# Kernel optimization log

Measured on AMD Instinct MI355X. Metric: run time of the kernel, lower is better.

The kernel has to match this reference:

```python
import jax, jax.numpy as jnp
import numpy as np
from jax import lax

BN_EPS = 1e-5


def _conv_bn_relu(x, W, b, gamma, beta):
    # x: [B, Cin, N]; W: [Cout, Cin]; 1x1 conv == channel GEMM
    y = jnp.einsum('oc,bcn->bon', W, x) + b[None, :, None]
    mean = jnp.mean(y, axis=(0, 2), keepdims=True)
    var = jnp.mean((y - mean) ** 2, axis=(0, 2), keepdims=True)  # biased, torch BN train mode
    y = gamma[None, :, None] * (y - mean) / jnp.sqrt(var + BN_EPS) + beta[None, :, None]
    return jax.nn.relu(y)


def setup_inputs() -> dict:
    key = jax.random.key(0)
    ks = jax.random.split(key, 8)
    B, N1, N2, C1, C2 = 16, 4096, 1024, 128, 256
    Cin, H = C1 + C2, 256  # MLP dims [384, 256, 256]
    inp = {
        'centroids1': jax.random.normal(ks[0], (B, 3, N1), jnp.float32),
        'centroids2': jax.random.normal(ks[1], (B, 3, N2), jnp.float32),
        'features1': jax.random.normal(ks[2], (B, C1, N1), jnp.float32),
        'features2': jax.random.normal(ks[3], (B, C2, N2), jnp.float32),
        'W1': jax.random.normal(ks[4], (H, Cin), jnp.float32) / np.sqrt(Cin),
        'b1': jnp.zeros((H,), jnp.float32),
        'g1': jnp.ones((H,), jnp.float32),
        'be1': jnp.zeros((H,), jnp.float32),
        'W2': jax.random.normal(ks[5], (H, H), jnp.float32) / np.sqrt(H),
        'b2': jnp.zeros((H,), jnp.float32),
        'g2': jnp.ones((H,), jnp.float32),
        'be2': jnp.zeros((H,), jnp.float32),
    }
    return inp


def reference(centroids1, centroids2, features1, features2,
              W1, b1, g1, be1, W2, b2, g2, be2):
    c1 = centroids1.transpose(0, 2, 1)  # [B, N1, 3]
    c2 = centroids2.transpose(0, 2, 1)  # [B, N2, 3]
    f2 = features2.transpose(0, 2, 1)   # [B, N2, C2]

    # pairwise squared distances [B, N1, N2]
    d = (jnp.sum(c1 ** 2, -1)[:, :, None] + jnp.sum(c2 ** 2, -1)[:, None, :]
         - 2.0 * jnp.einsum('bnd,bmd->bnm', c1, c2))

    # 3 nearest neighbors (smallest distances)
    neg_top, idx = lax.top_k(-d, 3)            # idx: [B, N1, 3]
    dist3 = -neg_top
    recip = 1.0 / (dist3 + 1e-8)
    weight = recip / jnp.sum(recip, axis=2, keepdims=True)  # [B, N1, 3]

    gathered = jax.vmap(lambda f, i: f[i])(f2, idx)         # [B, N1, 3, C2]
    interp = jnp.sum(gathered * weight[..., None], axis=2)  # [B, N1, C2]

    feats = jnp.concatenate((features1.transpose(0, 2, 1), interp), axis=-1)  # [B, N1, C1+C2]
    x = feats.transpose(0, 2, 1)  # [B, C1+C2, N1]
    x = _conv_bn_relu(x, W1, b1, g1, be1)
    x = _conv_bn_relu(x, W2, b2, g2, be2)
    return x  # [B, 256, N1]
```

## Files before the change

kernel.cpp:

```cpp
#include <hip/hip_runtime.h>
#include <math.h>

#define N1 4096
#define N2 1024
#define C1 128
#define C2 256
#define CIN 384
#define H 256
#define BATCH 16
#define BN_EPS 1e-5f

typedef __attribute__((ext_vector_type(8))) short bf16x8;
typedef __attribute__((ext_vector_type(4))) float f32x4;

__device__ inline float bf2f(short s) {
    union { unsigned u; float f; } x;
    x.u = ((unsigned)(unsigned short)s) << 16;
    return x.f;
}
__device__ inline short f2bf(float f) {
    union { float f; unsigned u; } x; x.f = f;
    unsigned r = x.u + 0x7fffu + ((x.u >> 16) & 1u);
    return (short)(r >> 16);
}

__global__ __launch_bounds__(256)
void knn_kernel(const float* __restrict__ c1, const float* __restrict__ c2,
                float4* __restrict__ pk) {
    __shared__ __align__(16) float4 sc[N2];
    __shared__ float md[64 * 13];
    __shared__ int   mi[64 * 13];
    const int b = blockIdx.y;
    const float* c2b = c2 + (size_t)b * 3 * N2;
    for (int j = threadIdx.x; j < N2; j += 256) {
        float xx = c2b[j], yy = c2b[N2 + j], zz = c2b[2 * N2 + j];
        sc[j] = make_float4(xx, yy, zz, xx * xx + yy * yy + zz * zz);
    }
    __syncthreads();

    const int t = threadIdx.x;
    const int q = t & 63;
    const int quarter = t >> 6;
    const int n = blockIdx.x * 64 + q;
    const float* c1b = c1 + (size_t)b * 3 * N1;
    const float x = c1b[n], y = c1b[N1 + n], z = c1b[2 * N1 + n];
    const float s1 = x * x + y * y + z * z;

    float d0 = 3.4e38f, d1 = 3.4e38f, d2 = 3.4e38f;
    int i0 = 0, i1 = 0, i2 = 0;
    const int j0 = quarter * 256;
    #pragma unroll 8
    for (int jj = 0; jj < 256; ++jj) {
        const int j = j0 + jj;
        float4 cc = sc[j];
        float dot = x * cc.x + y * cc.y + z * cc.z;
        float d = s1 + cc.w - 2.0f * dot;
        bool c0v = d < d0, c1v = d < d1, c2v = d < d2;
        i2 = c1v ? i1 : (c2v ? j : i2);
        i1 = c0v ? i0 : (c1v ? j : i1);
        i0 = c0v ? j  : i0;
        d2 = __builtin_amdgcn_fmed3f(d1, d2, d);
        d1 = __builtin_amdgcn_fmed3f(d0, d1, d);
        d0 = fminf(d0, d);
    }
    const int mb = q * 13 + quarter * 3;
    md[mb + 0] = d0; md[mb + 1] = d1; md[mb + 2] = d2;
    mi[mb + 0] = i0; mi[mb + 1] = i1; mi[mb + 2] = i2;
    __syncthreads();

    if (t < 64) {
        float e0 = 3.4e38f, e1 = 3.4e38f, e2 = 3.4e38f;
        int a0 = 0, a1 = 0, a2 = 0;
        #pragma unroll
        for (int r = 0; r < 12; ++r) {
            const int rr = t * 13 + (r / 3) * 3 + (r % 3);
            float d = md[rr]; int j = mi[rr];
            bool c0 = d < e0, c1v = d < e1, c2v = d < e2;
            e2 = c1v ? e1 : (c2v ? d : e2);  a2 = c1v ? a1 : (c2v ? j : a2);
            e1 = c0 ? e0 : (c1v ? d : e1);   a1 = c0 ? a0 : (c1v ? j : a1);
            e0 = c0 ? d  : e0;               a0 = c0 ? j  : a0;
        }
        float r0 = 1.0f / (e0 + 1e-8f);
        float r1 = 1.0f / (e1 + 1e-8f);
        float r2 = 1.0f / (e2 + 1e-8f);
        float rs = r0 + r1 + r2;
        unsigned pack = (unsigned)a0 | ((unsigned)a1 << 10) | ((unsigned)a2 << 20);
        pk[(size_t)b * N1 + n] = make_float4(__uint_as_float(pack), r0 / rs, r1 / rs, r2 / rs);
    }
}

__global__ __launch_bounds__(256)
void prep_w(const float* __restrict__ W, short* __restrict__ Wsw, int K) {
    const int nkb = K >> 3;
    const int id = blockIdx.x * 256 + threadIdx.x;
    if (id >= 256 * nkb) return;
    const int m = id / nkb, kb = id % nkb;
    const float* src = W + (size_t)m * K + kb * 8;
    bf16x8 v;
    #pragma unroll
    for (int j = 0; j < 8; ++j) v[j] = f2bf(src[j]);
    *(bf16x8*)(Wsw + ((size_t)kb * 256 + m) * 8) = v;
}

__global__ __launch_bounds__(256)
void transpose_f2(const float* __restrict__ f2, short* __restrict__ f2t) {
    __shared__ float st[32][33];
    const int j0 = blockIdx.x * 32, c0 = blockIdx.y * 32, b = blockIdx.z;
    const int t = threadIdx.x;
    {
        const int cc = t >> 3, jj = (t & 7) * 4;
        const float* src = f2 + ((size_t)b * C2 + c0 + cc) * N2 + j0 + jj;
        float4 v = *(const float4*)src;
        st[cc][jj + 0] = v.x; st[cc][jj + 1] = v.y;
        st[cc][jj + 2] = v.z; st[cc][jj + 3] = v.w;
    }
    __syncthreads();
    {
        const int j = t >> 3, cb = (t & 7) * 4;
        short4 v = { f2bf(st[cb + 0][j]), f2bf(st[cb + 1][j]),
                     f2bf(st[cb + 2][j]), f2bf(st[cb + 3][j]) };
        *(short4*)(f2t + ((size_t)b * N2 + j0 + j) * C2 + c0 + cb) = v;
    }
}

__global__ __launch_bounds__(256)
void prep_B1(const short* __restrict__ f2t, const float4* __restrict__ pk,
             short* __restrict__ B1) {
    const int b = blockIdx.y;
    const int n = blockIdx.x * 256 + threadIdx.x;
    float4 v = pk[(size_t)b * N1 + n];
    unsigned u = __float_as_uint(v.x);
    const short* r0 = f2t + ((size_t)b * N2 + (u & 1023u)) * C2;
    const short* r1 = f2t + ((size_t)b * N2 + ((u >> 10) & 1023u)) * C2;
    const short* r2 = f2t + ((size_t)b * N2 + ((u >> 20) & 1023u)) * C2;
    short* ob = B1 + ((size_t)b * 32 * N1 + n) * 8;
    #pragma unroll 4
    for (int kb = 0; kb < 32; ++kb) {
        bf16x8 g0 = *(const bf16x8*)(r0 + kb * 8);
        bf16x8 g1 = *(const bf16x8*)(r1 + kb * 8);
        bf16x8 g2 = *(const bf16x8*)(r2 + kb * 8);
        bf16x8 o;
        #pragma unroll
        for (int e = 0; e < 8; ++e)
            o[e] = f2bf(fmaf(v.w, bf2f(g2[e]), fmaf(v.z, bf2f(g1[e]), v.y * bf2f(g0[e]))));
        *(bf16x8*)(ob + (size_t)kb * N1 * 8) = o;
    }
}

template<int MODE>
__global__ __launch_bounds__(256, 4)
void gemm_kernel(const short* __restrict__ Wsw,
                 const float* __restrict__ f1, const short* __restrict__ Bkc,
                 const float* __restrict__ scale, const float* __restrict__ shift,
                 short* __restrict__ Ykc, float2* __restrict__ P) {
    __shared__ float sc_s[256], sh_s[256];
    __shared__ float2 pb[128][2];

    const int t = threadIdx.x;
    const int d = blockIdx.x;
    const int grp = d >> 4, rem = d & 15;
    const int mh = rem >> 3;
    const int pair = grp * 8 + (rem & 7);
    const int nt = pair & 31, b = pair >> 5;
    const int n0 = nt * 128;

    const int lane = t & 63, wv = t >> 6;
    const int wm = wv >> 1, wn = wv & 1;
    const int l16 = lane & 15, lq = lane >> 4;

    if (MODE == 1) {
        sc_s[t] = scale[t]; sh_s[t] = shift[t];
        __syncthreads();
    }

    const short* Bb = Bkc + (size_t)b * 32 * N1 * 8;
    const short* Abase = Wsw + ((size_t)lq * 256 + mh * 128 + wm * 64 + l16) * 8;
    const int nfr = n0 + wn * 64 + l16;

    f32x4 acc[4][4];
    #pragma unroll
    for (int i = 0; i < 4; ++i)
        #pragma unroll
        for (int j = 0; j < 4; ++j)
            acc[i][j] = (f32x4){0.f, 0.f, 0.f, 0.f};

    if (MODE == 0) {
        const float* f1b = f1 + (size_t)b * C1 * N1;
        #pragma unroll
        for (int s = 0; s < 4; ++s) {
            bf16x8 a[4], bv[4];
            const short* ap = Abase + (size_t)s * 4 * 256 * 8;
            #pragma unroll
            for (int f = 0; f < 4; ++f) a[f] = *(const bf16x8*)(ap + f * 16 * 8);
            const float* fp = f1b + (size_t)(s * 32 + lq * 8) * N1 + nfr;
            #pragma unroll
            for (int f = 0; f < 4; ++f) {
                #pragma unroll
                for (int e = 0; e < 8; ++e)
                    bv[f][e] = f2bf(fp[(size_t)e * N1 + f * 16]);
            }
            #pragma unroll
            for (int i = 0; i < 4; ++i)
                #pragma unroll
                for (int j = 0; j < 4; ++j)
                    acc[i][j] = __builtin_amdgcn_mfma_f32_16x16x32_bf16(a[i], bv[j], acc[i][j], 0, 0, 0);
        }
        #pragma unroll
        for (int s = 4; s < 12; ++s) {
            bf16x8 a[4], bv[4];
            const short* ap = Abase + (size_t)s * 4 * 256 * 8;
            #pragma unroll
            for (int f = 0; f < 4; ++f) a[f] = *(const bf16x8*)(ap + f * 16 * 8);
            const short* bp = Bb + ((size_t)(s * 4 + lq - 16) * N1 + nfr) * 8;
            #pragma unroll
            for (int f = 0; f < 4; ++f) bv[f] = *(const bf16x8*)(bp + f * 16 * 8);
            #pragma unroll
            for (int i = 0; i < 4; ++i)
                #pragma unroll
                for (int j = 0; j < 4; ++j)
                    acc[i][j] = __builtin_amdgcn_mfma_f32_16x16x32_bf16(a[i], bv[j], acc[i][j], 0, 0, 0);
        }
    } else {
        #pragma unroll
        for (int s = 0; s < 8; ++s) {
            bf16x8 a[4], raw[4], bv[4];
            const short* ap = Abase + (size_t)s * 4 * 256 * 8;
            #pragma unroll
            for (int f = 0; f < 4; ++f) a[f] = *(const bf16x8*)(ap + f * 16 * 8);
            const short* bp = Bb + ((size_t)(s * 4 + lq) * N1 + nfr) * 8;
            #pragma unroll
            for (int f = 0; f < 4; ++f) raw[f] = *(const bf16x8*)(bp + f * 16 * 8);
            const int k0 = s * 32 + lq * 8;
            float sck[8], shk[8];
            #pragma unroll
            for (int e = 0; e < 8; ++e) { sck[e] = sc_s[k0 + e]; shk[e] = sh_s[k0 + e]; }
            #pragma unroll
            for (int f = 0; f < 4; ++f)
                #pragma unroll
                for (int e = 0; e < 8; ++e)
                    bv[f][e] = f2bf(fmaxf(fmaf(bf2f(raw[f][e]), sck[e], shk[e]), 0.f));
            #pragma unroll
            for (int i = 0; i < 4; ++i)
                #pragma unroll
                for (int j = 0; j < 4; ++j)
                    acc[i][j] = __builtin_amdgcn_mfma_f32_16x16x32_bf16(a[i], bv[j], acc[i][j], 0, 0, 0);
        }
    }

    short* Yb = Ykc + (size_t)b * 32 * N1 * 8;
    #pragma unroll
    for (int i = 0; i < 4; ++i) {
        const int kb = mh * 16 + wm * 8 + i * 2 + (lq >> 1);
        const int kr0 = (lq & 1) * 4;
        #pragma unroll
        for (int j = 0; j < 4; ++j) {
            const int n = n0 + wn * 64 + j * 16 + l16;
            short4 v = { f2bf(acc[i][j][0]), f2bf(acc[i][j][1]),
                         f2bf(acc[i][j][2]), f2bf(acc[i][j][3]) };
            *(short4*)(Yb + ((size_t)kb * N1 + n) * 8 + kr0) = v;
        }
    }

    #pragma unroll
    for (int i = 0; i < 4; ++i) {
        #pragma unroll
        for (int r = 0; r < 4; ++r) {
            float s = 0.f, qq = 0.f;
            #pragma unroll
            for (int j = 0; j < 4; ++j) {
                float xv = acc[i][j][r];
                s += xv; qq += xv * xv;
            }
            #pragma unroll
            for (int msk = 1; msk < 16; msk <<= 1) {
                s  += __shfl_xor(s, msk);
                qq += __shfl_xor(qq, msk);
            }
            if (l16 == 0)
                pb[wm * 64 + i * 16 + lq * 4 + r][wn] = make_float2(s, qq);
        }
    }
    __syncthreads();
    if (t < 128) {
        float2 a = pb[t][0], c = pb[t][1];
        P[(size_t)(mh * 128 + t) * 512 + b * 32 + nt] = make_float2(a.x + c.x, a.y + c.y);
    }
}

__global__ __launch_bounds__(256)
void bn_reduce(const float2* __restrict__ P, const float* __restrict__ g,
               const float* __restrict__ be, float* __restrict__ scale,
               float* __restrict__ shift) {
    const int c = blockIdx.x, t = threadIdx.x;
    float2 v0 = P[(size_t)c * 512 + t];
    float2 v1 = P[(size_t)c * 512 + 256 + t];
    float s = v0.x + v1.x, q = v0.y + v1.y;
    __shared__ float ss[256], sq[256];
    ss[t] = s; sq[t] = q;
    __syncthreads();
    for (int o = 128; o > 0; o >>= 1) {
        if (t < o) { ss[t] += ss[t + o]; sq[t] += sq[t + o]; }
        __syncthreads();
    }
    if (t == 0) {
        const float inv = 1.0f / (float)(BATCH * N1);
        float mean = ss[0] * inv;
        float var  = sq[0] * inv - mean * mean;
        float sc = g[c] / sqrtf(var + BN_EPS);
        scale[c] = sc;
        shift[c] = be[c] - mean * sc;
    }
}

__global__ __launch_bounds__(256)
void final_bn_relu(const short* __restrict__ y2kc, const float* __restrict__ scale,
                   const float* __restrict__ shift, float* __restrict__ out) {
    const int t = threadIdx.x;
    const int n0 = blockIdx.x * 1024 + t * 4;
    const int kb = blockIdx.y, b = blockIdx.z;
    const short* src = y2kc + ((size_t)(b * 32 + kb) * N1 + n0) * 8;
    bf16x8 v0 = *(const bf16x8*)(src);
    bf16x8 v1 = *(const bf16x8*)(src + 8);
    bf16x8 v2 = *(const bf16x8*)(src + 16);
    bf16x8 v3 = *(const bf16x8*)(src + 24);
    #pragma unroll
    for (int e = 0; e < 8; ++e) {
        const float sc = scale[kb * 8 + e], sh = shift[kb * 8 + e];
        float4 o;
        o.x = fmaxf(fmaf(bf2f(v0[e]), sc, sh), 0.f);
        o.y = fmaxf(fmaf(bf2f(v1[e]), sc, sh), 0.f);
        o.z = fmaxf(fmaf(bf2f(v2[e]), sc, sh), 0.f);
        o.w = fmaxf(fmaf(bf2f(v3[e]), sc, sh), 0.f);
        *(float4*)(out + ((size_t)(b * 256 + kb * 8 + e) * N1) + n0) = o;
    }
}

extern "C" void kernel_launch(void* const* d_in, const int* in_sizes, int n_in,
                              void* d_out, int out_size, void* d_ws, size_t ws_size,
                              hipStream_t stream) {
    const float* c1  = (const float*)d_in[0];
    const float* c2  = (const float*)d_in[1];
    const float* f1  = (const float*)d_in[2];
    const float* f2  = (const float*)d_in[3];
    const float* W1  = (const float*)d_in[4];
    const float* g1  = (const float*)d_in[6];
    const float* be1 = (const float*)d_in[7];
    const float* W2  = (const float*)d_in[8];
    const float* g2  = (const float*)d_in[10];
    const float* be2 = (const float*)d_in[11];
    float* out = (float*)d_out;

    char* ws = (char*)d_ws;
    short*  B1   = (short*)ws;
    short*  y2kc = (short*)ws;
    short*  f2t  = (short*)(ws + (32u << 20));
    short*  y1kc = (short*)(ws + (32u << 20));
    short*  W1s  = (short*)(ws + (64u << 20));
    short*  W2s  = (short*)(ws + (64u << 20) + (256u << 10));
    float4* pk   = (float4*)(ws + (64u << 20) + (512u << 10));
    float2* P    = (float2*)(ws + (64u << 20) + (512u << 10) + (1u << 20));
    float* scale1 = (float*)(ws + (64u << 20) + (512u << 10) + (2u << 20));
    float* shift1 = scale1 + 256;
    float* scale2 = shift1 + 256;
    float* shift2 = scale2 + 256;

    prep_w<<<48, 256, 0, stream>>>(W1, W1s, CIN);
    prep_w<<<32, 256, 0, stream>>>(W2, W2s, H);
    transpose_f2<<<dim3(N2 / 32, C2 / 32, BATCH), 256, 0, stream>>>(f2, f2t);
    knn_kernel<<<dim3(N1 / 64, BATCH), 256, 0, stream>>>(c1, c2, pk);
    prep_B1<<<dim3(N1 / 256, BATCH), 256, 0, stream>>>(f2t, pk, B1);

    gemm_kernel<0><<<1024, 256, 0, stream>>>(
        W1s, f1, B1, nullptr, nullptr, y1kc, P);
    bn_reduce<<<256, 256, 0, stream>>>(P, g1, be1, scale1, shift1);

    gemm_kernel<1><<<1024, 256, 0, stream>>>(
        W2s, nullptr, y1kc, scale1, shift1, y2kc, P);
    bn_reduce<<<256, 256, 0, stream>>>(P, g2, be2, scale2, shift2);

    final_bn_relu<<<dim3(N1 / 1024, 32, BATCH), 256, 0, stream>>>(y2kc, scale2, shift2, out);
}
```

Before: 151.4 us.

## Stage GEMM operands through double-buffered LDS with async global-to-LDS loads

After: 165.6 us. +9.4%, slower.

```diff
diff --git a/kernel.cpp b/kernel.cpp
--- a/kernel.cpp
+++ b/kernel.cpp
@@ -22,6 +22,12 @@
     union { float f; unsigned u; } x; x.f = f;
     unsigned r = x.u + 0x7fffu + ((x.u >> 16) & 1u);
     return (short)(r >> 16);
+}
+
+typedef const __attribute__((address_space(1))) unsigned int guint;
+typedef __attribute__((address_space(3))) unsigned int luint;
+__device__ inline void gll16(const void* g, void* l) {
+    __builtin_amdgcn_global_load_lds((guint*)g, (luint*)l, 16, 0, 0);
 }
 
 __global__ __launch_bounds__(256)
@@ -148,12 +154,15 @@
 }
 
 template<int MODE>
-__global__ __launch_bounds__(256, 4)
+__global__ __launch_bounds__(256)
 void gemm_kernel(const short* __restrict__ Wsw,
                  const float* __restrict__ f1, const short* __restrict__ Bkc,
-                 const float* __restrict__ scale, const float* __restrict__ shift,
                  short* __restrict__ Ykc, float2* __restrict__ P) {
-    __shared__ float sc_s[256], sh_s[256];
+    constexpr int K = (MODE == 0) ? CIN : H;
+    constexpr int NT = K / 32;
+
+    __shared__ __align__(16) short A_lds[2][4][128][8];
+    __shared__ __align__(16) short B_lds[2][4][128][8];
     __shared__ float2 pb[128][2];
 
     const int t = threadIdx.x;
@@ -168,14 +177,11 @@
     const int wm = wv >> 1, wn = wv & 1;
     const int l16 = lane & 15, lq = lane >> 4;
 
-    if (MODE == 1) {
-        sc_s[t] = scale[t]; sh_s[t] = shift[t];
-        __syncthreads();
-    }
-
+    const float* f1b = (MODE == 0) ? f1 + (size_t)b * C1 * N1 : (const float*)nullptr;
     const short* Bb = Bkc + (size_t)b * 32 * N1 * 8;
-    const short* Abase = Wsw + ((size_t)lq * 256 + mh * 128 + wm * 64 + l16) * 8;
-    const int nfr = n0 + wn * 64 + l16;
+
+    const int skb = t >> 7;
+    const int sn0 = t & 127;
 
     f32x4 acc[4][4];
     #pragma unroll
@@ -184,67 +190,85 @@
         for (int j = 0; j < 4; ++j)
             acc[i][j] = (f32x4){0.f, 0.f, 0.f, 0.f};
 
+    auto stageA = [&](int step, int bufi) {
+        #pragma unroll
+        for (int i = 0; i < 2; ++i) {
+            const int u0 = i * 256 + wv * 64;
+            const int kb = u0 >> 7, m0 = u0 & 127;
+            const short* g = Wsw + (((size_t)step * 4 + kb) * 256 + mh * 128 + m0 + lane) * 8;
+            gll16(g, &A_lds[bufi][0][0][0] + (size_t)u0 * 8);
+        }
+    };
+    auto stageB_gll = [&](int kbg, int bufi) {
+        #pragma unroll
+        for (int i = 0; i < 2; ++i) {
+            const int u0 = i * 256 + wv * 64;
+            const int kb = u0 >> 7, nn = u0 & 127;
+            const short* g = Bb + (((size_t)(kbg + kb)) * N1 + n0 + nn + lane) * 8;
+            gll16(g, &B_lds[bufi][0][0][0] + (size_t)u0 * 8);
+        }
+    };
+
+    float pf[16];
+    auto loadF1 = [&](int step) {
+        #pragma unroll
+        for (int h = 0; h < 2; ++h) {
+            const int kb = skb + h * 2;
+            const float* src = f1b + (size_t)(step * 32 + kb * 8) * N1 + n0 + sn0;
+            #pragma unroll
+            for (int e = 0; e < 8; ++e) pf[h * 8 + e] = src[(size_t)e * N1];
+        }
+    };
+    auto writeF1 = [&](int bufi) {
+        #pragma unroll
+        for (int h = 0; h < 2; ++h) {
+            const int kb = skb + h * 2;
+            bf16x8 pv;
+            #pragma unroll
+            for (int e = 0; e < 8; ++e) pv[e] = f2bf(pf[h * 8 + e]);
+            *(bf16x8*)&B_lds[bufi][kb][sn0][0] = pv;
+        }
+    };
+
+    auto compute = [&](int bufi) {
+        bf16x8 a[4], bb[4];
+        #pragma unroll
+        for (int f = 0; f < 4; ++f) {
+            a[f]  = *(const bf16x8*)&A_lds[bufi][lq][wm * 64 + f * 16 + l16][0];
+            bb[f] = *(const bf16x8*)&B_lds[bufi][lq][wn * 64 + f * 16 + l16][0];
+        }
+        #pragma unroll
+        for (int i = 0; i < 4; ++i)
+            #pragma unroll
+            for (int j = 0; j < 4; ++j)
+                acc[i][j] = __builtin_amdgcn_mfma_f32_16x16x32_bf16(a[i], bb[j], acc[i][j], 0, 0, 0);
+    };
+
     if (MODE == 0) {
-        const float* f1b = f1 + (size_t)b * C1 * N1;
-        #pragma unroll
-        for (int s = 0; s < 4; ++s) {
-            bf16x8 a[4], bv[4];
-            const short* ap = Abase + (size_t)s * 4 * 256 * 8;
-            #pragma unroll
-            for (int f = 0; f < 4; ++f) a[f] = *(const bf16x8*)(ap + f * 16 * 8);
-            const float* fp = f1b + (size_t)(s * 32 + lq * 8) * N1 + nfr;
-            #pragma unroll
-            for (int f = 0; f < 4; ++f) {
-                #pragma unroll
-                for (int e = 0; e < 8; ++e)
-                    bv[f][e] = f2bf(fp[(size_t)e * N1 + f * 16]);
-            }
-            #pragma unroll
-            for (int i = 0; i < 4; ++i)
-                #pragma unroll
-                for (int j = 0; j < 4; ++j)
-                    acc[i][j] = __builtin_amdgcn_mfma_f32_16x16x32_bf16(a[i], bv[j], acc[i][j], 0, 0, 0);
-        }
-        #pragma unroll
-        for (int s = 4; s < 12; ++s) {
-            bf16x8 a[4], bv[4];
-            const short* ap = Abase + (size_t)s * 4 * 256 * 8;
-            #pragma unroll
-            for (int f = 0; f < 4; ++f) a[f] = *(const bf16x8*)(ap + f * 16 * 8);
-            const short* bp = Bb + ((size_t)(s * 4 + lq - 16) * N1 + nfr) * 8;
-            #pragma unroll
-            for (int f = 0; f < 4; ++f) bv[f] = *(const bf16x8*)(bp + f * 16 * 8);
-            #pragma unroll
-            for (int i = 0; i < 4; ++i)
-                #pragma unroll
-                for (int j = 0; j < 4; ++j)
-                    acc[i][j] = __builtin_amdgcn_mfma_f32_16x16x32_bf16(a[i], bv[j], acc[i][j], 0, 0, 0);
-        }
+        loadF1(0);
+        stageA(0, 0);
+        writeF1(0);
     } else {
-        #pragma unroll
-        for (int s = 0; s < 8; ++s) {
-            bf16x8 a[4], raw[4], bv[4];
-            const short* ap = Abase + (size_t)s * 4 * 256 * 8;
-            #pragma unroll
-            for (int f = 0; f < 4; ++f) a[f] = *(const bf16x8*)(ap + f * 16 * 8);
-            const short* bp = Bb + ((size_t)(s * 4 + lq) * N1 + nfr) * 8;
-            #pragma unroll
-            for (int f = 0; f < 4; ++f) raw[f] = *(const bf16x8*)(bp + f * 16 * 8);
-            const int k0 = s * 32 + lq * 8;
-            float sck[8], shk[8];
-            #pragma unroll
-            for (int e = 0; e < 8; ++e) { sck[e] = sc_s[k0 + e]; shk[e] = sh_s[k0 + e]; }
-            #pragma unroll
-            for (int f = 0; f < 4; ++f)
-                #pragma unroll
-                for (int e = 0; e < 8; ++e)
-                    bv[f][e] = f2bf(fmaxf(fmaf(bf2f(raw[f][e]), sck[e], shk[e]), 0.f));
-            #pragma unroll
-            for (int i = 0; i < 4; ++i)
-                #pragma unroll
-                for (int j = 0; j < 4; ++j)
-                    acc[i][j] = __builtin_amdgcn_mfma_f32_16x16x32_bf16(a[i], bv[j], acc[i][j], 0, 0, 0);
-        }
+        stageA(0, 0);
+        stageB_gll(0, 0);
+    }
+    __syncthreads();
+
+    int buf = 0;
+    #pragma unroll
+    for (int s = 0; s < NT; ++s) {
+        const int sx = s + 1;
+        const bool has_next = (sx < NT);
+        const bool next_reg = (MODE == 0) && (sx < 4);
+        if (has_next) {
+            if (next_reg) loadF1(sx);
+            stageA(sx, buf ^ 1);
+            if (!next_reg) stageB_gll(MODE == 0 ? (sx * 4 - 16) : sx * 4, buf ^ 1);
+        }
+        compute(buf);
+        if (has_next && next_reg) writeF1(buf ^ 1);
+        __syncthreads();
+        buf ^= 1;
     }
 
     short* Yb = Ykc + (size_t)b * 32 * N1 * 8;
@@ -313,6 +337,19 @@
 }
 
 __global__ __launch_bounds__(256)
+void bn_apply(const short* __restrict__ yin, const float* __restrict__ scale,
+              const float* __restrict__ shift, short* __restrict__ yout) {
+    const int i8 = blockIdx.x * 256 + threadIdx.x;
+    bf16x8 v = ((const bf16x8*)yin)[i8];
+    const int c0 = ((i8 >> 12) & 31) * 8;
+    bf16x8 o;
+    #pragma unroll
+    for (int e = 0; e < 8; ++e)
+        o[e] = f2bf(fmaxf(fmaf(bf2f(v[e]), scale[c0 + e], shift[c0 + e]), 0.f));
+    ((bf16x8*)yout)[i8] = o;
+}
+
+__global__ __launch_bounds__(256)
 void final_bn_relu(const short* __restrict__ y2kc, const float* __restrict__ scale,
                    const float* __restrict__ shift, float* __restrict__ out) {
     const int t = threadIdx.x;
@@ -352,9 +389,10 @@
 
     char* ws = (char*)d_ws;
     short*  B1   = (short*)ws;
-    short*  y2kc = (short*)ws;
+    short*  y1r  = (short*)ws;
     short*  f2t  = (short*)(ws + (32u << 20));
     short*  y1kc = (short*)(ws + (32u << 20));
+    short*  y2kc = (short*)(ws + (32u << 20));
     short*  W1s  = (short*)(ws + (64u << 20));
     short*  W2s  = (short*)(ws + (64u << 20) + (256u << 10));
     float4* pk   = (float4*)(ws + (64u << 20) + (512u << 10));
@@ -370,12 +408,11 @@
     knn_kernel<<<dim3(N1 / 64, BATCH), 256, 0, stream>>>(c1, c2, pk);
     prep_B1<<<dim3(N1 / 256, BATCH), 256, 0, stream>>>(f2t, pk, B1);
 
-    gemm_kernel<0><<<1024, 256, 0, stream>>>(
-        W1s, f1, B1, nullptr, nullptr, y1kc, P);
+    gemm_kernel<0><<<1024, 256, 0, stream>>>(W1s, f1, B1, y1kc, P);
     bn_reduce<<<256, 256, 0, stream>>>(P, g1, be1, scale1, shift1);
-
-    gemm_kernel<1><<<1024, 256, 0, stream>>>(
-        W2s, nullptr, y1kc, scale1, shift1, y2kc, P);
+    bn_apply<<<8192, 256, 0, stream>>>(y1kc, scale1, shift1, y1r);
+
+    gemm_kernel<1><<<1024, 256, 0, stream>>>(W2s, nullptr, y1r, y2kc, P);
     bn_reduce<<<256, 256, 0, stream>>>(P, g2, be2, scale2, shift2);
 
     final_bn_relu<<<dim3(N1 / 1024, 32, BATCH), 256, 0, stream>>>(y2kc, scale2, shift2, out);
```
